# Optimization experiments

Hardware: AMD Instinct MI355X
Metric: run time of the kernel (lower is better)

The kernel has to match this reference:

```python
import jax, jax.numpy as jnp
import numpy as np

EMBED_DIM = 1024
NUM_HEADS = 16
MICRO_HEADS = 8
HEAD_DIM = EMBED_DIM // NUM_HEADS
N_BLOCKS = NUM_HEADS // MICRO_HEADS
B, N = 2, 2048


def setup_inputs() -> dict:
    key = jax.random.key(0)
    ks = jax.random.split(key, 9)
    s = 1.0 / np.sqrt(EMBED_DIM)
    return {
        "x": jax.random.normal(ks[0], (B, N, EMBED_DIM), dtype=jnp.float32),
        "Wq": jax.random.uniform(ks[1], (EMBED_DIM, EMBED_DIM), jnp.float32, -s, s),
        "bq": jax.random.uniform(ks[2], (EMBED_DIM,), jnp.float32, -s, s),
        "Wk": jax.random.uniform(ks[3], (EMBED_DIM, EMBED_DIM), jnp.float32, -s, s),
        "bk": jax.random.uniform(ks[4], (EMBED_DIM,), jnp.float32, -s, s),
        "Wv": jax.random.uniform(ks[5], (EMBED_DIM, EMBED_DIM), jnp.float32, -s, s),
        "bv": jax.random.uniform(ks[6], (EMBED_DIM,), jnp.float32, -s, s),
        "Wo": jax.random.uniform(ks[7], (EMBED_DIM, EMBED_DIM), jnp.float32, -s, s),
        "bo": jax.random.uniform(ks[8], (EMBED_DIM,), jnp.float32, -s, s),
    }


def _scramble(t, b, n):
    # Replicates torch's Qh[:, :, hs:he, :].contiguous().view(B*mh, N, dh)
    # which is a raw row-major reshape mixing (N, mh) -> (mh, N) per batch.
    # (B, N, E) -> (B, N, nb, mh, dh) -> (B, nb, N, mh, dh) -> raw reshape -> (B, nb, mh, N, dh)
    t = t.reshape(b, n, N_BLOCKS, MICRO_HEADS, HEAD_DIM)
    t = jnp.transpose(t, (0, 2, 1, 3, 4))
    return t.reshape(b, N_BLOCKS, MICRO_HEADS, n, HEAD_DIM)


def reference(x, Wq, bq, Wk, bk, Wv, bv, Wo, bo):
    b, n, e = x.shape
    scale = HEAD_DIM ** -0.5
    Q = x @ Wq.T + bq
    K = x @ Wk.T + bk
    V = x @ Wv.T + bv
    q = _scramble(Q, b, n)  # (B, nb, mh, N, dh)
    k = _scramble(K, b, n)
    v = _scramble(V, b, n)
    s = jnp.einsum("bgmqd,bgmkd->bgmqk", q, k) * scale  # (B, nb, mh, N, N)
    causal = jnp.tril(jnp.ones((n, n), dtype=bool))
    s = jnp.where(causal, s, -jnp.inf)
    p = jax.nn.softmax(s, axis=-1)
    ctx = jnp.einsum("bgmqk,bgmkd->bgmqd", p, v)  # (B, nb, mh, N, dh)
    # inverse raw reshape: (mh, N, dh) -> (N, mh*dh) per (b, g), then concat blocks
    ctx = ctx.reshape(b, N_BLOCKS, n, MICRO_HEADS * HEAD_DIM)
    ctx = jnp.transpose(ctx, (0, 2, 1, 3)).reshape(b, n, e)
    return ctx @ Wo.T + bo
```

## Files before the change

### kernel.cpp

```cpp
#include <hip/hip_runtime.h>
#include <hip/hip_bf16.h>


typedef unsigned short ushortT;
typedef __attribute__((ext_vector_type(8))) short short8;
typedef __attribute__((ext_vector_type(4))) float floatx4;
typedef __attribute__((ext_vector_type(2))) unsigned int uintx2;

__device__ inline void gl_lds16(const ushortT* g, ushortT* lds) {
    __builtin_amdgcn_global_load_lds(
        (const __attribute__((address_space(1))) unsigned int*)g,
        (__attribute__((address_space(3))) unsigned int*)lds, 16, 0, 0);
}

__global__ __launch_bounds__(256) void cvt_bf16(
    const float* __restrict__ x,
    const float* __restrict__ Wq, const float* __restrict__ Wk,
    const float* __restrict__ Wv, const float* __restrict__ Wo,
    ushortT* __restrict__ xb, ushortT* __restrict__ Wb)
{
    const unsigned tid = blockIdx.x * 256 + threadIdx.x;
    const size_t e = (size_t)tid * 8;
    const float* src;
    ushortT* dst;
    size_t off;
    if (e < (size_t)(4u << 20)) { src = x; dst = xb; off = e; }
    else {
        const size_t r = e - (size_t)(4u << 20);
        const int wsel = (int)(r >> 20);
        off = r & 0xFFFFFu;
        src = (wsel == 0) ? Wq : (wsel == 1) ? Wk : (wsel == 2) ? Wv : Wo;
        dst = Wb + ((size_t)wsel << 20);
    }
    const float4 f0 = ((const float4*)(src + off))[0];
    const float4 f1 = ((const float4*)(src + off))[1];
    union { __hip_bfloat162 h[4]; uint4 u; } pk;
    pk.h[0] = __float22bfloat162_rn(float2{f0.x, f0.y});
    pk.h[1] = __float22bfloat162_rn(float2{f0.z, f0.w});
    pk.h[2] = __float22bfloat162_rn(float2{f1.x, f1.y});
    pk.h[3] = __float22bfloat162_rn(float2{f1.z, f1.w});
    *(uint4*)(dst + off) = pk.u;
}

__global__ __launch_bounds__(512, 2) void gemm_qkv_8p(
    const ushortT* __restrict__ A, const ushortT* __restrict__ Wst,
    const float* __restrict__ b0, const float* __restrict__ b1, const float* __restrict__ b2,
    ushortT* __restrict__ O0, ushortT* __restrict__ O1, ushortT* __restrict__ O2)
{
    __shared__ __align__(16) ushortT sm[65536];

    const int t = threadIdx.x;
    const int bid = blockIdx.x;
    const int wg = (bid & 7) * 24 + (bid >> 3);
    const int mt = wg / 12;
    const int nt = wg - mt * 12;
    const int m0 = mt * 256;
    const int mat = nt >> 2;
    const int n0 = (nt & 3) * 256;
    const ushortT* W = Wst + ((size_t)mat << 20);
    const float* bias = (mat == 0) ? b0 : (mat == 1) ? b1 : b2;
    ushortT* Out     = (mat == 0) ? O0 : (mat == 1) ? O1 : O2;
    const float oscale = (mat == 0) ? 0.18033688f : 1.0f;

    const int w = t >> 6, lane = t & 63;
    const int wm = w >> 2, wn = w & 3;
    const int col16 = lane & 15, quad = lane >> 4;
    const int c7 = col16 & 7;

    const int ko[2] = { ((0 + quad) ^ c7) << 3, ((4 + quad) ^ c7) << 3 };
    const int xbase = (wm * 128 + col16) * 64;
    const int wbase = (wn * 64 + col16) * 64;

    const int trow = t >> 3;
    const int sch = (t & 7) ^ (trow & 7);
    const ushortT* gA[4]; const ushortT* gB[4];
    #pragma unroll
    for (int q = 0; q < 4; q++) {
        gA[q] = A + (size_t)(m0 + q * 64 + trow) * 1024 + sch * 8;
        gB[q] = W + (size_t)(n0 + q * 64 + trow) * 1024 + sch * 8;
    }
    const int dst0 = (w << 6) * 8;

    floatx4 acc[8][4];
    #pragma unroll
    for (int i = 0; i < 8; i++)
        #pragma unroll
        for (int j = 0; j < 4; j++) acc[i][j] = (floatx4)0.0f;

    auto issue8 = [&](const int ab, const int bb) {
        #pragma unroll
        for (int q = 0; q < 4; q++) {
            gl_lds16(gA[q], sm + ab + dst0 + q * 4096);
            gl_lds16(gB[q], sm + bb + dst0 + q * 4096);
            gA[q] += 64; gB[q] += 64;
        }
    };

    auto group = [&](const int ab, const int bb) {
        short8 bw[4];
        #pragma unroll
        for (int ks = 0; ks < 2; ks++) {
            #pragma unroll
            for (int mh = 0; mh < 2; mh++) {
                short8 bx[4];
                if (mh == 0) {
                    #pragma unroll
                    for (int nf = 0; nf < 4; nf++)
                        bw[nf] = *(const short8*)(sm + bb + wbase + nf * 1024 + ko[ks]);
                }
                #pragma unroll
                for (int j = 0; j < 4; j++)
                    bx[j] = *(const short8*)(sm + ab + xbase + (mh * 4 + j) * 1024 + ko[ks]);
                __builtin_amdgcn_s_barrier();
                __builtin_amdgcn_s_setprio(1);
                #pragma unroll
                for (int j = 0; j < 4; j++)
                    #pragma unroll
                    for (int nf = 0; nf < 4; nf++)
                        acc[mh * 4 + j][nf] = __builtin_amdgcn_mfma_f32_16x16x32_bf16(
                            bw[nf], bx[j], acc[mh * 4 + j][nf], 0, 0, 0);
                __builtin_amdgcn_s_setprio(0);
                __builtin_amdgcn_s_barrier();
            }
        }
    };

    issue8(0, 16384);
    issue8(32768, 49152);

    #pragma unroll 1
    for (int it = 0; it < 7; ++it) {
        asm volatile("s_waitcnt vmcnt(8)" ::: "memory");
        __builtin_amdgcn_s_barrier();
        group(0, 16384);
        issue8(0, 16384);
        asm volatile("s_waitcnt vmcnt(8)" ::: "memory");
        __builtin_amdgcn_s_barrier();
        group(32768, 49152);
        issue8(32768, 49152);
    }
    asm volatile("s_waitcnt vmcnt(8)" ::: "memory");
    __builtin_amdgcn_s_barrier();
    group(0, 16384);
    asm volatile("s_waitcnt vmcnt(0)" ::: "memory");
    __builtin_amdgcn_s_barrier();
    group(32768, 49152);

    #pragma unroll
    for (int mf = 0; mf < 8; mf++) {
        const int m = m0 + wm * 128 + mf * 16 + col16;
        #pragma unroll
        for (int nf = 0; nf < 4; nf++) {
            const int nb = n0 + wn * 64 + nf * 16 + quad * 4;
            const float4 bv4 = *(const float4*)(bias + nb);
            const float v0 = (acc[mf][nf][0] + bv4.x) * oscale;
            const float v1 = (acc[mf][nf][1] + bv4.y) * oscale;
            const float v2 = (acc[mf][nf][2] + bv4.z) * oscale;
            const float v3 = (acc[mf][nf][3] + bv4.w) * oscale;
            union { __hip_bfloat162 h[2]; unsigned long long u; } pk2;
            pk2.h[0] = __float22bfloat162_rn(float2{v0, v1});
            pk2.h[1] = __float22bfloat162_rn(float2{v2, v3});
            *(unsigned long long*)(Out + (size_t)m * 1024 + nb) = pk2.u;
        }
    }
}

template <bool OUT_F32, bool N64>
__global__ __launch_bounds__(256) void gemm_lds(
    const ushortT* __restrict__ A, const ushortT* __restrict__ Wst,
    const float* __restrict__ b0, const float* __restrict__ b1, const float* __restrict__ b2,
    void* __restrict__ O0, void* __restrict__ O1, void* __restrict__ O2)
{
    constexpr int NT = N64 ? 64 : 128;
    constexpr int NJ = N64 ? 2 : 4;
    constexpr int WQ = N64 ? 2 : 4;
    __shared__ __align__(16) ushortT As[128 * 64];
    __shared__ __align__(16) ushortT Bs[NT * 64];
    const int t = threadIdx.x;
    const int m0 = blockIdx.y * 128;
    const int n0g = blockIdx.x * NT;
    const int mat = n0g >> 10;
    const int n0 = n0g & 1023;
    const ushortT* W = Wst + ((size_t)mat << 20);
    const float* bias = (mat == 0) ? b0 : (mat == 1) ? b1 : b2;
    void* Out        = (mat == 0) ? O0 : (mat == 1) ? O1 : O2;

    const int w = t >> 6, lane = t & 63;
    const int wm = w >> 1, wn = w & 1;
    const int col16 = lane & 15, quad = lane >> 4;

    floatx4 acc[4][NJ];
    for (int i = 0; i < 4; i++)
        for (int j = 0; j < NJ; j++) acc[i][j] = (floatx4)0.0f;

    const int cid0 = w * (N64 ? 128 : 256) + lane;

    for (int k0 = 0; k0 < 1024; k0 += 64) {
        #pragma unroll
        for (int q = 0; q < 4; q++) {
            const int cid = w * 256 + q * 64 + lane;
            const int row = cid >> 3;
            const int sch = (cid & 7) ^ (row & 7);
            gl_lds16(A + (size_t)(m0 + row) * 1024 + k0 + sch * 8,
                     As + (size_t)(w * 256 + q * 64) * 8);
        }
        #pragma unroll
        for (int q = 0; q < WQ; q++) {
            const int cid = cid0 + q * 64;
            const int row = cid >> 3;
            const int sch = (cid & 7) ^ (row & 7);
            gl_lds16(W + (size_t)(n0 + row) * 1024 + k0 + sch * 8,
                     Bs + (size_t)(w * (N64 ? 128 : 256) + q * 64) * 8);
        }
        __syncthreads();
        #pragma unroll
        for (int ks = 0; ks < 64; ks += 32) {
            const int cbase = (ks >> 3) + quad;
            const int sw = col16 & 7;
            short8 a[4], b[NJ];
            #pragma unroll
            for (int i = 0; i < 4; i++) {
                const int row = wm * 64 + i * 16 + col16;
                a[i] = *(const short8*)(As + row * 64 + ((cbase ^ sw) << 3));
            }
            #pragma unroll
            for (int j = 0; j < NJ; j++) {
                const int row = wn * (NT / 2) + j * 16 + col16;
                b[j] = *(const short8*)(Bs + row * 64 + ((cbase ^ sw) << 3));
            }
            #pragma unroll
            for (int i = 0; i < 4; i++)
                #pragma unroll
                for (int j = 0; j < NJ; j++)
                    acc[i][j] = __builtin_amdgcn_mfma_f32_16x16x32_bf16(b[j], a[i], acc[i][j], 0, 0, 0);
        }
        __syncthreads();
    }

    #pragma unroll
    for (int i = 0; i < 4; i++) {
        const int m = m0 + wm * 64 + i * 16 + col16;
        #pragma unroll
        for (int j = 0; j < NJ; j++) {
            const int nb = n0 + wn * (NT / 2) + j * 16 + quad * 4;
            const float4 bv4 = *(const float4*)(bias + nb);
            const float v0 = acc[i][j][0] + bv4.x;
            const float v1 = acc[i][j][1] + bv4.y;
            const float v2 = acc[i][j][2] + bv4.z;
            const float v3 = acc[i][j][3] + bv4.w;
            if constexpr (OUT_F32) {
                *(float4*)((float*)Out + (size_t)m * 1024 + nb) = float4{v0, v1, v2, v3};
            } else {
                union { __hip_bfloat162 h[2]; unsigned long long u; } pk2;
                pk2.h[0] = __float22bfloat162_rn(float2{v0, v1});
                pk2.h[1] = __float22bfloat162_rn(float2{v2, v3});
                *(unsigned long long*)((ushortT*)Out + (size_t)m * 1024 + nb) = pk2.u;
            }
        }
    }
}

__global__ __launch_bounds__(256) void transpose_v(
    const ushortT* __restrict__ Vb, ushortT* __restrict__ VT)
{
    __shared__ ushortT L[64 * 65];
    const int bid = blockIdx.x;
    const int pt = bid & 31, s = bid >> 5;
    const int bb = s >> 4, g = (s >> 3) & 1, mh = s & 7;
    const size_t baseoff = (size_t)bb * 2048 * 1024 + (size_t)g * 512;
    const int t = threadIdx.x;
    {
        const int pr = t >> 2, seg = t & 3;
        const int i = mh * 2048 + pt * 64 + pr;
        const uint4* src = (const uint4*)(Vb + baseoff + (size_t)(i >> 3) * 1024 + (i & 7) * 64 + seg * 16);
        union { uint4 u[2]; ushortT h[16]; } tmp;
        tmp.u[0] = src[0]; tmp.u[1] = src[1];
        #pragma unroll
        for (int d = 0; d < 16; d++) L[pr * 65 + seg * 16 + d] = tmp.h[d];
    }
    __syncthreads();
    {
        const int dc = t >> 2, pseg = t & 3;
        union { uint4 u[2]; ushortT h[16]; } tmp;
        #pragma unroll
        for (int j = 0; j < 16; j++) tmp.h[j] = L[(pseg * 16 + j) * 65 + dc];
        uint4* dst = (uint4*)(VT + (size_t)s * 64 * 2048 + (size_t)dc * 2048 + pt * 64 + pseg * 16);
        dst[0] = tmp.u[0]; dst[1] = tmp.u[1];
    }
}

__global__ __launch_bounds__(256) void attn(
    const ushortT* __restrict__ Qb, const ushortT* __restrict__ Kb,
    const ushortT* __restrict__ VT, ushortT* __restrict__ Cb)
{
    __shared__ __align__(16) ushortT lds[16384];

    const int t = threadIdx.x;
    const int bid = blockIdx.x;
    const int xcd = bid & 7;
    const int u = bid >> 3;
    const int s = xcd * 4 + (u & 3);
    const int x5 = u >> 2;
    const int qt = (x5 < 8) ? x5 : (x5 < 16) ? (39 - x5)
                 : (x5 < 24) ? (x5 - 8) : (47 - x5);
    const int bb = s >> 4, g = (s >> 3) & 1, mh = s & 7;

    const int w = t >> 6, lane = t & 63;
    const int col16 = lane & 15, quad = lane >> 4;

    const size_t baseoff = (size_t)bb * 2048 * 1024 + (size_t)g * 512;
    const size_t vtbase  = (size_t)s * 64 * 2048;
    const int i0 = mh * 2048 + qt * 64;
    const int qloc = w * 16 + col16;
    const int c7 = col16 & 7;

    short8 qreg[2];
    {
        const int i = i0 + qloc;
        const ushortT* p = Qb + baseoff + (size_t)(i >> 3) * 1024 + (i & 7) * 64;
        qreg[0] = *(const short8*)(p + quad * 8);
        qreg[1] = *(const short8*)(p + 32 + quad * 8);
    }

    int kbo[2];
    kbo[0] = col16 * 64 + (((0 + quad) ^ c7) << 3);
    kbo[1] = col16 * 64 + (((4 + quad) ^ c7) << 3);

    const int cid0 = w * 128 + lane, cid1 = cid0 + 64;
    const int row0 = cid0 >> 3, sch0 = (cid0 & 7) ^ (row0 & 7);
    const int row1 = cid1 >> 3, sch1 = (cid1 & 7) ^ (row1 & 7);
    const int jr0 = mh * 2048 + row0;
    const int jr1 = mh * 2048 + row1;
    const ushortT* gk0 = Kb + baseoff + (size_t)(jr0 >> 3) * 1024 + (jr0 & 7) * 64 + sch0 * 8;
    const ushortT* gk1 = Kb + baseoff + (size_t)(jr1 >> 3) * 1024 + (jr1 & 7) * 64 + sch1 * 8;
    const ushortT* gv0 = VT + vtbase + (size_t)row0 * 2048 + sch0 * 8;
    const ushortT* gv1 = VT + vtbase + (size_t)row1 * 2048 + sch1 * 8;
    const int sdK = w * 1024;

    auto stage = [&](int sb) {
        gl_lds16(gk0, lds + sb + sdK);
        gl_lds16(gk1, lds + sb + sdK + 512);
        gl_lds16(gv0, lds + sb + 8192 + sdK);
        gl_lds16(gv1, lds + sb + 8192 + sdK + 512);
        gk0 += 8192; gk1 += 8192; gv0 += 64; gv1 += 64;
    };

    float l4[4] = {0.f, 0.f, 0.f, 0.f};
    floatx4 Oacc[4];
    for (int c = 0; c < 4; c++) Oacc[c] = (floatx4)0.0f;

    stage(0);
    int sb = 4096;
    for (int kt = 0; kt <= qt; ++kt) {
        __syncthreads();
        if (kt < qt) { stage(sb); sb ^= 4096; }

        floatx4 sc[4];
        for (int c = 0; c < 4; c++) sc[c] = (floatx4)0.0f;
        #pragma unroll
        for (int h = 0; h < 2; h++) {
            const short8 bq = qreg[h];
            #pragma unroll
            for (int c = 0; c < 4; c++) {
                const short8 ak = *(const short8*)(lds + kbo[h] + c * 1024);
                sc[c] = __builtin_amdgcn_mfma_f32_16x16x32_bf16(ak, bq, sc[c], 0, 0, 0);
            }
        }

        if (kt == qt) {
            #pragma unroll
            for (int c = 0; c < 4; c++)
                #pragma unroll
                for (int r = 0; r < 4; r++)
                    if ((c * 16 + quad * 4 + r) > qloc) sc[c][r] = -1e30f;
        }

        unsigned pw[4][2];
        #pragma unroll
        for (int c = 0; c < 4; c++) {
            float pv0 = __builtin_amdgcn_exp2f(sc[c][0]);
            float pv1 = __builtin_amdgcn_exp2f(sc[c][1]);
            float pv2 = __builtin_amdgcn_exp2f(sc[c][2]);
            float pv3 = __builtin_amdgcn_exp2f(sc[c][3]);
            l4[0] += pv0; l4[1] += pv1; l4[2] += pv2; l4[3] += pv3;
            union { __hip_bfloat162 h; unsigned u; } a, b;
            a.h = __float22bfloat162_rn(float2{pv0, pv1});
            b.h = __float22bfloat162_rn(float2{pv2, pv3});
            pw[c][0] = a.u; pw[c][1] = b.u;
        }

        #pragma unroll
        for (int h = 0; h < 2; h++) {
            unsigned dw[4];
            #pragma unroll
            for (int uu = 0; uu < 2; uu++) {
                uintx2 s32 = __builtin_amdgcn_permlane32_swap(pw[2 * h][uu], pw[2 * h + 1][uu], false, false);
                uintx2 s16 = __builtin_amdgcn_permlane16_swap(s32.x, s32.y, false, false);
                dw[uu] = s16.x; dw[2 + uu] = s16.y;
            }
            union { unsigned u[4]; short8 s; } bpu;
            bpu.u[0] = dw[0]; bpu.u[1] = dw[1]; bpu.u[2] = dw[2]; bpu.u[3] = dw[3];
            const short8 bp = bpu.s;
            #pragma unroll
            for (int c = 0; c < 4; c++) {
                const short8 av = *(const short8*)(lds + kbo[h] + 8192 + c * 1024);
                Oacc[c] = __builtin_amdgcn_mfma_f32_16x16x32_bf16(av, bp, Oacc[c], 0, 0, 0);
            }
        }

        kbo[0] ^= 4096; kbo[1] ^= 4096;
    }

    float l_s = (l4[0] + l4[1]) + (l4[2] + l4[3]);
    l_s += __shfl_xor(l_s, 16);
    l_s += __shfl_xor(l_s, 32);

    {
        const int i = i0 + qloc;
        const float inv = 1.0f / l_s;
        ushortT* dst = Cb + baseoff + (size_t)(i >> 3) * 1024 + (i & 7) * 64;
        #pragma unroll
        for (int c = 0; c < 4; c++) {
            union { __hip_bfloat162 h[2]; unsigned long long u; } pk2;
            pk2.h[0] = __float22bfloat162_rn(float2{Oacc[c][0] * inv, Oacc[c][1] * inv});
            pk2.h[1] = __float22bfloat162_rn(float2{Oacc[c][2] * inv, Oacc[c][3] * inv});
            *(unsigned long long*)(dst + c * 16 + quad * 4) = pk2.u;
        }
    }
}

extern "C" void kernel_launch(void* const* d_in, const int* in_sizes, int n_in,
                              void* d_out, int out_size, void* d_ws, size_t ws_size,
                              hipStream_t stream)
{
    const float* x  = (const float*)d_in[0];
    const float* Wq = (const float*)d_in[1];
    const float* bq = (const float*)d_in[2];
    const float* Wk = (const float*)d_in[3];
    const float* bk = (const float*)d_in[4];
    const float* Wv = (const float*)d_in[5];
    const float* bv = (const float*)d_in[6];
    const float* Wo = (const float*)d_in[7];
    const float* bo = (const float*)d_in[8];

    const size_t M1 = (size_t)1024 * 1024;
    ushortT* Wb  = (ushortT*)d_ws;
    ushortT* xb  = Wb + 4 * M1;
    ushortT* Qb  = xb + 4 * M1;
    ushortT* Kb  = Qb + 4 * M1;
    ushortT* Vb  = (ushortT*)d_out;
    ushortT* VTb = xb;
    ushortT* Cb  = Qb;

    dim3 blk(256);
    cvt_bf16<<<dim3(4096), blk, 0, stream>>>(x, Wq, Wk, Wv, Wo, xb, Wb);
    gemm_qkv_8p<<<dim3(192), dim3(512), 0, stream>>>(
        xb, Wb, bq, bk, bv, Qb, Kb, Vb);
    transpose_v<<<dim3(1024), blk, 0, stream>>>(Vb, VTb);
    attn<<<dim3(1024), blk, 0, stream>>>(Qb, Kb, VTb, Cb);
    gemm_lds<true, true><<<dim3(16, 32), blk, 0, stream>>>(
        Cb, Wb + 3 * M1, bo, bo, bo, d_out, d_out, d_out);
}
```

Measured before the change: 184.0 us.

## Fuse V transpose into QKV GEMM epilogue via LDS staging

Removes the separate transpose_v kernel by having the V-projection tiles of the QKV GEMM stage their bf16 outputs in shared memory in transposed (scrambled) order and write VT directly. This avoids one kernel launch plus a full write and re-read of the V matrix through global memory. In exchange, the V blocks get a heavier epilogue with scalar LDS stores (possible bank conflicts) and extra barriers, and VT is moved to a new workspace region.

After: 178.5 us. 3.0% less time.

```diff
diff --git a/kernel.cpp b/kernel.cpp
--- a/kernel.cpp
+++ b/kernel.cpp
@@ -1,11 +1,16 @@
 #include <hip/hip_runtime.h>
 #include <hip/hip_bf16.h>
-
 
 typedef unsigned short ushortT;
 typedef __attribute__((ext_vector_type(8))) short short8;
 typedef __attribute__((ext_vector_type(4))) float floatx4;
 typedef __attribute__((ext_vector_type(2))) unsigned int uintx2;
+
+__device__ inline ushortT f2bf(float f) {
+    union { float f; unsigned int i; } v; v.f = f;
+    unsigned int x = v.i;
+    return (ushortT)((x + 0x7fffu + ((x >> 16) & 1u)) >> 16);
+}
 
 __device__ inline void gl_lds16(const ushortT* g, ushortT* lds) {
     __builtin_amdgcn_global_load_lds(
@@ -45,7 +50,7 @@
 __global__ __launch_bounds__(512, 2) void gemm_qkv_8p(
     const ushortT* __restrict__ A, const ushortT* __restrict__ Wst,
     const float* __restrict__ b0, const float* __restrict__ b1, const float* __restrict__ b2,
-    ushortT* __restrict__ O0, ushortT* __restrict__ O1, ushortT* __restrict__ O2)
+    ushortT* __restrict__ O0, ushortT* __restrict__ O1, ushortT* __restrict__ VT)
 {
     __shared__ __align__(16) ushortT sm[65536];
 
@@ -59,7 +64,7 @@
     const int n0 = (nt & 3) * 256;
     const ushortT* W = Wst + ((size_t)mat << 20);
     const float* bias = (mat == 0) ? b0 : (mat == 1) ? b1 : b2;
-    ushortT* Out     = (mat == 0) ? O0 : (mat == 1) ? O1 : O2;
+    ushortT* Out     = (mat == 0) ? O0 : O1;
     const float oscale = (mat == 0) ? 0.18033688f : 1.0f;
 
     const int w = t >> 6, lane = t & 63;
@@ -146,21 +151,51 @@
     __builtin_amdgcn_s_barrier();
     group(32768, 49152);
 
-    #pragma unroll
-    for (int mf = 0; mf < 8; mf++) {
-        const int m = m0 + wm * 128 + mf * 16 + col16;
-        #pragma unroll
-        for (int nf = 0; nf < 4; nf++) {
-            const int nb = n0 + wn * 64 + nf * 16 + quad * 4;
-            const float4 bv4 = *(const float4*)(bias + nb);
-            const float v0 = (acc[mf][nf][0] + bv4.x) * oscale;
-            const float v1 = (acc[mf][nf][1] + bv4.y) * oscale;
-            const float v2 = (acc[mf][nf][2] + bv4.z) * oscale;
-            const float v3 = (acc[mf][nf][3] + bv4.w) * oscale;
-            union { __hip_bfloat162 h[2]; unsigned long long u; } pk2;
-            pk2.h[0] = __float22bfloat162_rn(float2{v0, v1});
-            pk2.h[1] = __float22bfloat162_rn(float2{v2, v3});
-            *(unsigned long long*)(Out + (size_t)m * 1024 + nb) = pk2.u;
+    if (mat != 2) {
+        #pragma unroll
+        for (int mf = 0; mf < 8; mf++) {
+            const int m = m0 + wm * 128 + mf * 16 + col16;
+            #pragma unroll
+            for (int nf = 0; nf < 4; nf++) {
+                const int nb = n0 + wn * 64 + nf * 16 + quad * 4;
+                const float4 bv4 = *(const float4*)(bias + nb);
+                const float v0 = (acc[mf][nf][0] + bv4.x) * oscale;
+                const float v1 = (acc[mf][nf][1] + bv4.y) * oscale;
+                const float v2 = (acc[mf][nf][2] + bv4.z) * oscale;
+                const float v3 = (acc[mf][nf][3] + bv4.w) * oscale;
+                union { __hip_bfloat162 h[2]; unsigned long long u; } pk2;
+                pk2.h[0] = __float22bfloat162_rn(float2{v0, v1});
+                pk2.h[1] = __float22bfloat162_rn(float2{v2, v3});
+                *(unsigned long long*)(Out + (size_t)m * 1024 + nb) = pk2.u;
+            }
+        }
+    } else {
+        __syncthreads();
+        #pragma unroll
+        for (int mf = 0; mf < 8; mf++) {
+            const int ml = wm * 128 + mf * 16 + col16;
+            const int pib = ml * 4 + wn;
+            #pragma unroll
+            for (int nf = 0; nf < 4; nf++) {
+                const int dbase = nf * 16 + quad * 4;
+                const float4 bv4 = *(const float4*)(bias + n0 + wn * 64 + dbase);
+                sm[(dbase + 0) * 1024 + pib] = f2bf(acc[mf][nf][0] + bv4.x);
+                sm[(dbase + 1) * 1024 + pib] = f2bf(acc[mf][nf][1] + bv4.y);
+                sm[(dbase + 2) * 1024 + pib] = f2bf(acc[mf][nf][2] + bv4.z);
+                sm[(dbase + 3) * 1024 + pib] = f2bf(acc[mf][nf][3] + bv4.w);
+            }
+        }
+        __syncthreads();
+        const int b2 = mt >> 3, mhh = mt & 7, gg = n0 >> 9;
+        const int p0 = (n0 & 511) >> 6;
+        ushortT* vbase = VT + (size_t)((b2 * 2 + gg) * 8 + mhh) * 131072 + p0;
+        #pragma unroll
+        for (int v = 0; v < 32; v++) {
+            const int e = v * 512 + t;
+            const int d = e >> 8;
+            const int runml = e & 255;
+            const uint2 val = *(const uint2*)(sm + d * 1024 + runml * 4);
+            *(uint2*)(vbase + d * 2048 + runml * 8) = val;
         }
     }
 }
@@ -260,35 +295,6 @@
     }
 }
 
-__global__ __launch_bounds__(256) void transpose_v(
-    const ushortT* __restrict__ Vb, ushortT* __restrict__ VT)
-{
-    __shared__ ushortT L[64 * 65];
-    const int bid = blockIdx.x;
-    const int pt = bid & 31, s = bid >> 5;
-    const int bb = s >> 4, g = (s >> 3) & 1, mh = s & 7;
-    const size_t baseoff = (size_t)bb * 2048 * 1024 + (size_t)g * 512;
-    const int t = threadIdx.x;
-    {
-        const int pr = t >> 2, seg = t & 3;
-        const int i = mh * 2048 + pt * 64 + pr;
-        const uint4* src = (const uint4*)(Vb + baseoff + (size_t)(i >> 3) * 1024 + (i & 7) * 64 + seg * 16);
-        union { uint4 u[2]; ushortT h[16]; } tmp;
-        tmp.u[0] = src[0]; tmp.u[1] = src[1];
-        #pragma unroll
-        for (int d = 0; d < 16; d++) L[pr * 65 + seg * 16 + d] = tmp.h[d];
-    }
-    __syncthreads();
-    {
-        const int dc = t >> 2, pseg = t & 3;
-        union { uint4 u[2]; ushortT h[16]; } tmp;
-        #pragma unroll
-        for (int j = 0; j < 16; j++) tmp.h[j] = L[(pseg * 16 + j) * 65 + dc];
-        uint4* dst = (uint4*)(VT + (size_t)s * 64 * 2048 + (size_t)dc * 2048 + pt * 64 + pseg * 16);
-        dst[0] = tmp.u[0]; dst[1] = tmp.u[1];
-    }
-}
-
 __global__ __launch_bounds__(256) void attn(
     const ushortT* __restrict__ Qb, const ushortT* __restrict__ Kb,
     const ushortT* __restrict__ VT, ushortT* __restrict__ Cb)
@@ -448,15 +454,13 @@
     ushortT* xb  = Wb + 4 * M1;
     ushortT* Qb  = xb + 4 * M1;
     ushortT* Kb  = Qb + 4 * M1;
-    ushortT* Vb  = (ushortT*)d_out;
-    ushortT* VTb = xb;
+    ushortT* VTb = Wb + 16 * M1;
     ushortT* Cb  = Qb;
 
     dim3 blk(256);
     cvt_bf16<<<dim3(4096), blk, 0, stream>>>(x, Wq, Wk, Wv, Wo, xb, Wb);
     gemm_qkv_8p<<<dim3(192), dim3(512), 0, stream>>>(
-        xb, Wb, bq, bk, bv, Qb, Kb, Vb);
-    transpose_v<<<dim3(1024), blk, 0, stream>>>(Vb, VTb);
+        xb, Wb, bq, bk, bv, Qb, Kb, VTb);
     attn<<<dim3(1024), blk, 0, stream>>>(Qb, Kb, VTb, Cb);
     gemm_lds<true, true><<<dim3(16, 32), blk, 0, stream>>>(
         Cb, Wb + 3 * M1, bo, bo, bo, d_out, d_out, d_out);
```
